# Performance work log

Measured on AMD Instinct MI355X. Metric: run time of the kernel, lower is better.

## Reference

```python
import jax, jax.numpy as jnp
import numpy as np

EPS = 1e-5

def _ln(x, g, b):
    m = x.mean(-1, keepdims=True)
    v = x.var(-1, keepdims=True)
    return (x - m) / jnp.sqrt(v + EPS) * g + b

def _ln_na(x):
    m = x.mean(-1, keepdims=True)
    v = x.var(-1, keepdims=True)
    return (x - m) / jnp.sqrt(v + EPS)

def setup_inputs() -> dict:
    key = jax.random.key(0)
    ks = jax.random.split(key, 12)
    B, J, D, H, E, Z = 128, 4096, 64, 128, 256, 32
    s = 0.05
    return {
        "x": jax.random.normal(ks[0], (B, J), jnp.float32),
        "mask": jax.random.randint(ks[1], (B, J), 0, 2, jnp.int32),
        "feature_embedding": jax.random.normal(ks[2], (J, D), jnp.float32),
        "hW1": jax.random.normal(ks[3], (1 + D, H), jnp.float32) * s,
        "hb1": jnp.zeros((H,), jnp.float32),
        "hg1": jnp.ones((H,), jnp.float32),
        "hbt1": jnp.zeros((H,), jnp.float32),
        "hW2": jax.random.normal(ks[4], (H, D), jnp.float32) * s,
        "hb2": jnp.zeros((D,), jnp.float32),
        "hg2": jnp.ones((D,), jnp.float32),
        "hbt2": jnp.zeros((D,), jnp.float32),
        "eW1": jax.random.normal(ks[5], (D, E), jnp.float32) * s,
        "eb1": jnp.zeros((E,), jnp.float32),
        "eW2": jax.random.normal(ks[6], (E, 2 * Z), jnp.float32) * s,
        "eb2": jnp.zeros((2 * Z,), jnp.float32),
    }

def reference(x, mask, feature_embedding, hW1, hb1, hg1, hbt1, hW2, hb2, hg2, hbt2, eW1, eb1, eW2, eb2):
    B, J = x.shape
    D = feature_embedding.shape[1]
    m = (mask > 0).astype(x.dtype)  # (B, J)
    # per-(b,j) MLP on [x_bj, F_j]; masked entries are zeroed before pooling,
    # which equals the original gather-then-MLP-then-sum over observed entries.
    F = jnp.broadcast_to(feature_embedding[None], (B, J, D))
    h_in = jnp.concatenate([x[..., None], F], axis=-1)        # (B, J, 1+D)
    h = jax.nn.relu(_ln(h_in @ hW1 + hb1, hg1, hbt1))          # (B, J, H)
    h = jax.nn.relu(_ln(h @ hW2 + hb2, hg2, hbt2))             # (B, J, D)
    pooled = jnp.einsum('bjd,bj->bd', h, m)                    # sum over observed
    cnt = jnp.maximum(m.sum(-1, keepdims=True), 1.0)
    c = pooled / cnt                                           # mean pool; zeros if no obs
    # FCLayers (2 layers, LayerNorm w/o affine, ReLU each layer)
    e = jax.nn.relu(_ln_na(c @ eW1 + eb1))                     # (B, E)
    out = jax.nn.relu(_ln_na(e @ eW2 + eb2))                   # (B, 2Z)
    mu, logvar = jnp.split(out, 2, axis=-1)
    return (mu, logvar)
```

## Files before the change

### kernel.cpp

```cpp
#include <hip/hip_runtime.h>
#include <hip/hip_bf16.h>

#define B_  128
#define J_  4096
#define D_  64
#define H_  128
#define E_  256
#define Z_  32

typedef __attribute__((ext_vector_type(8))) short short8;
typedef __attribute__((ext_vector_type(4))) float floatx4;

#define OFF_G      0u
#define OFF_GSTATS 2097152u
#define OFF_SCAL   2162688u
#define OFF_W0C    2162944u
#define OFF_C3     2163456u
#define OFF_W2F    2163968u
#define OFF_POOL   2180352u

#if defined(__has_builtin)
#if __has_builtin(__builtin_amdgcn_cvt_pk_bf16_f32)
#define HAVE_CVT_PK_BF16 1
#endif
#endif

#ifdef HAVE_CVT_PK_BF16
static __device__ __forceinline__ unsigned pk2(float a, float b) {
    return __builtin_bit_cast(unsigned, __builtin_amdgcn_cvt_pk_bf16_f32(a, b));
}
#else
static __device__ __forceinline__ unsigned pk2(float a, float b) {
    __hip_bfloat162 t = __float22bfloat162_rn(make_float2(a, b));
    union { __hip_bfloat162 h; unsigned u; } c; c.h = t; return c.u;
}
#endif

__global__ __launch_bounds__(128) void pre_kernel(
    const float* __restrict__ F, const float* __restrict__ hW1,
    const float* __restrict__ hb1, const float* __restrict__ hg1,
    const float* __restrict__ hbt1, const float* __restrict__ hW2,
    float* __restrict__ Gp, float4* __restrict__ Gstats,
    float* __restrict__ scal, float* __restrict__ w0c, float* __restrict__ c3,
    uint4* __restrict__ w2f, float4* __restrict__ zero4)
{
    __shared__ float red[24];
    const int bid = blockIdx.x;
    const int t = threadIdx.x;

    if (bid > 1024) {
        const int base = (bid - 1025) * 256;
        zero4[base + t]       = make_float4(0.f, 0.f, 0.f, 0.f);
        zero4[base + 128 + t] = make_float4(0.f, 0.f, 0.f, 0.f);
        return;
    }

    if (bid == 1024) {
        const float w0h = hW1[t];
        float s = w0h, q = w0h * w0h;
#pragma unroll
        for (int off = 32; off; off >>= 1) {
            s += __shfl_xor(s, off);
            q += __shfl_xor(q, off);
        }
        if ((t & 63) == 0) { red[(t >> 6) * 2] = s; red[(t >> 6) * 2 + 1] = q; }
        __syncthreads();
        const float mw0  = (red[0] + red[2]) * (1.f / (float)H_);
        const float ew02 = (red[1] + red[3]) * (1.f / (float)H_);
        if (t == 0) { scal[0] = mw0; scal[1] = ew02; }
        w0c[t] = (hW1[t] - mw0) * hg1[t];
        c3[t]  = hbt1[t];

        const int lane = t & 63, half = t >> 6;
        const int quad = lane >> 4, col = lane & 15;
        for (int f = half; f < 16; f += 2) {
            const int kstep = f >> 2, nt = f & 3;
            const int kbase = kstep * 32 + quad * 8;
            const int n = nt * 16 + col;
            unsigned r[4];
#pragma unroll
            for (int p = 0; p < 4; p++)
                r[p] = pk2(hW2[(kbase + 2*p) * D_ + n], hW2[(kbase + 2*p + 1) * D_ + n]);
            w2f[f * 64 + lane] = make_uint4(r[0], r[1], r[2], r[3]);
        }
        return;
    }

    const int j0 = bid * 4;
    const int h  = t;
    const float* f0 = F + (size_t)(j0 + 0) * D_;
    const float* f1 = F + (size_t)(j0 + 1) * D_;
    const float* f2p = F + (size_t)(j0 + 2) * D_;
    const float* f3 = F + (size_t)(j0 + 3) * D_;
    const float bias = hb1[h];
    float a0 = bias, a1 = bias, a2 = bias, a3 = bias;
#pragma unroll
    for (int d = 0; d < D_; d++) {
        const float w = hW1[(d + 1) * H_ + h];
        a0 = fmaf(f0[d], w, a0);
        a1 = fmaf(f1[d], w, a1);
        a2 = fmaf(f2p[d], w, a2);
        a3 = fmaf(f3[d], w, a3);
    }

    const float w0h = hW1[h];
    const float g1h = hg1[h];
    float accs[4] = {a0, a1, a2, a3};
#pragma unroll
    for (int q = 0; q < 4; q++) {
        float s1 = accs[q], s2 = w0h * accs[q], s3 = accs[q] * accs[q];
#pragma unroll
        for (int off = 32; off; off >>= 1) {
            s1 += __shfl_xor(s1, off);
            s2 += __shfl_xor(s2, off);
            s3 += __shfl_xor(s3, off);
        }
        if ((h & 63) == 0) {
            int w = h >> 6;
            red[q*6 + w*3 + 0] = s1; red[q*6 + w*3 + 1] = s2; red[q*6 + w*3 + 2] = s3;
        }
    }
    __syncthreads();
    const float inv = 1.f / (float)H_;
#pragma unroll
    for (int q = 0; q < 4; q++) {
        const float mG = (red[q*6 + 0] + red[q*6 + 3]) * inv;
        if (h == 0)
            Gstats[j0 + q] = make_float4(mG, (red[q*6+1] + red[q*6+4]) * inv,
                                             (red[q*6+2] + red[q*6+5]) * inv, 0.f);
        Gp[(j0 + q) * H_ + h] = (accs[q] - mG) * g1h;
    }
}

#define TPW 2
#define BB  4

__global__ __launch_bounds__(256, 2) void main_kernel(
    const float* __restrict__ x, const int* __restrict__ mask,
    const float* __restrict__ Gp, const float4* __restrict__ Gstats,
    const float* __restrict__ scal,
    const float* __restrict__ w0c, const float* __restrict__ c3,
    const uint4* __restrict__ w2f,
    const float* __restrict__ hb2, const float* __restrict__ hg2,
    const float* __restrict__ hbt2,
    float* __restrict__ pooled)
{
    const int tid  = threadIdx.x;
    const int lane = tid & 63;
    const int wv   = tid >> 6;
    const int quad = lane >> 4;
    const int col  = lane & 15;
    const int b0   = blockIdx.y * BB;

    short8 w2r[16];
#pragma unroll
    for (int f = 0; f < 16; f++) {
        union { uint4 v; short8 s; } c; c.v = w2f[f * 64 + lane];
        w2r[f] = c.s;
    }
    float4 wc[4][2], cc[4][2];
#pragma unroll
    for (int k = 0; k < 4; k++) {
        wc[k][0] = ((const float4*)(w0c + k*32 + quad*8))[0];
        wc[k][1] = ((const float4*)(w0c + k*32 + quad*8))[1];
        cc[k][0] = ((const float4*)(c3  + k*32 + quad*8))[0];
        cc[k][1] = ((const float4*)(c3  + k*32 + quad*8))[1];
    }
    float hb2v[4], g2v[4], bt2v[4];
#pragma unroll
    for (int nt = 0; nt < 4; nt++) {
        hb2v[nt] = hb2[nt*16 + col];
        g2v[nt]  = hg2[nt*16 + col];
        bt2v[nt] = hbt2[nt*16 + col];
    }
    const float mw0s  = scal[0];
    const float ew02s = scal[1];

    float pool[BB][4];
#pragma unroll
    for (int bb = 0; bb < BB; bb++)
#pragma unroll
        for (int nt = 0; nt < 4; nt++) pool[bb][nt] = 0.f;

    for (int t = 0; t < TPW; t++) {
        const int tIdx = (blockIdx.x * 4 + wv) * TPW + t;
        const int j0   = tIdx * 16;
        const int rowA = j0 + col;

        const float4 gs = Gstats[rowA];
        float xv[BB]; int4 mk[BB];
#pragma unroll
        for (int bb = 0; bb < BB; bb++) {
            xv[bb] = x[(size_t)(b0 + bb) * J_ + rowA];
            mk[bb] = *(const int4*)(mask + (size_t)(b0 + bb) * J_ + j0 + quad * 4);
        }
        const float* gpr = Gp + rowA * H_ + quad * 8;
        float4 ga[4][2];
#pragma unroll
        for (int k = 0; k < 4; k++) {
            ga[k][0] = ((const float4*)(gpr + k*32))[0];
            ga[k][1] = ((const float4*)(gpr + k*32))[1];
        }

#pragma unroll
        for (int bb = 0; bb < BB; bb++) {
            const float xA = xv[bb];
            const float mean = fmaf(xA, mw0s, gs.x);
            const float eh2  = fmaf(xA, fmaf(xA, ew02s, 2.f * gs.y), gs.z);
            const float r1   = rsqrtf(fmaf(-mean, mean, eh2) + 1e-5f);

            floatx4 acc[4];
#pragma unroll
            for (int nt = 0; nt < 4; nt++) acc[nt] = (floatx4){0.f, 0.f, 0.f, 0.f};

#pragma unroll
            for (int k = 0; k < 4; k++) {
                const float h0 = fmaxf(0.f, fmaf(fmaf(xA, wc[k][0].x, ga[k][0].x), r1, cc[k][0].x));
                const float h1 = fmaxf(0.f, fmaf(fmaf(xA, wc[k][0].y, ga[k][0].y), r1, cc[k][0].y));
                const float h2 = fmaxf(0.f, fmaf(fmaf(xA, wc[k][0].z, ga[k][0].z), r1, cc[k][0].z));
                const float h3 = fmaxf(0.f, fmaf(fmaf(xA, wc[k][0].w, ga[k][0].w), r1, cc[k][0].w));
                const float h4 = fmaxf(0.f, fmaf(fmaf(xA, wc[k][1].x, ga[k][1].x), r1, cc[k][1].x));
                const float h5 = fmaxf(0.f, fmaf(fmaf(xA, wc[k][1].y, ga[k][1].y), r1, cc[k][1].y));
                const float h6 = fmaxf(0.f, fmaf(fmaf(xA, wc[k][1].z, ga[k][1].z), r1, cc[k][1].z));
                const float h7 = fmaxf(0.f, fmaf(fmaf(xA, wc[k][1].w, ga[k][1].w), r1, cc[k][1].w));
                union { unsigned u[4]; short8 s; } af;
                af.u[0] = pk2(h0, h1);
                af.u[1] = pk2(h2, h3);
                af.u[2] = pk2(h4, h5);
                af.u[3] = pk2(h6, h7);
                acc[0] = __builtin_amdgcn_mfma_f32_16x16x32_bf16(af.s, w2r[k*4+0], acc[0], 0, 0, 0);
                acc[1] = __builtin_amdgcn_mfma_f32_16x16x32_bf16(af.s, w2r[k*4+1], acc[1], 0, 0, 0);
                acc[2] = __builtin_amdgcn_mfma_f32_16x16x32_bf16(af.s, w2r[k*4+2], acc[2], 0, 0, 0);
                acc[3] = __builtin_amdgcn_mfma_f32_16x16x32_bf16(af.s, w2r[k*4+3], acc[3], 0, 0, 0);
            }

            float sa[4], qa[4];
#pragma unroll
            for (int r = 0; r < 4; r++) {
                const float v0 = acc[0][r] + hb2v[0];
                const float v1 = acc[1][r] + hb2v[1];
                const float v2 = acc[2][r] + hb2v[2];
                const float v3 = acc[3][r] + hb2v[3];
                acc[0][r] = v0; acc[1][r] = v1; acc[2][r] = v2; acc[3][r] = v3;
                sa[r] = (v0 + v1) + (v2 + v3);
                qa[r] = fmaf(v0, v0, fmaf(v1, v1, fmaf(v2, v2, v3 * v3)));
            }
#pragma unroll
            for (int m = 1; m < 16; m <<= 1) {
#pragma unroll
                for (int r = 0; r < 4; r++) {
                    sa[r] += __shfl_xor(sa[r], m);
                    qa[r] += __shfl_xor(qa[r], m);
                }
            }
            float mrr[4];
            mrr[0] = (mk[bb].x > 0) ? 1.f : 0.f;
            mrr[1] = (mk[bb].y > 0) ? 1.f : 0.f;
            mrr[2] = (mk[bb].z > 0) ? 1.f : 0.f;
            mrr[3] = (mk[bb].w > 0) ? 1.f : 0.f;
#pragma unroll
            for (int r = 0; r < 4; r++) {
                const float m2 = sa[r] * (1.f / 64.f);
                const float v2 = fmaf(-m2, m2, qa[r] * (1.f / 64.f));
                const float r2 = rsqrtf(v2 + 1e-5f);
#pragma unroll
                for (int nt = 0; nt < 4; nt++) {
                    const float rg  = r2 * g2v[nt];
                    const float off = fmaf(-m2, rg, bt2v[nt]);
                    const float o   = fmaxf(0.f, fmaf(acc[nt][r], rg, off));
                    pool[bb][nt] = fmaf(mrr[r], o, pool[bb][nt]);
                }
            }
        }
    }

#pragma unroll
    for (int m = 16; m < 64; m <<= 1)
#pragma unroll
        for (int bb = 0; bb < BB; bb++)
#pragma unroll
            for (int nt = 0; nt < 4; nt++)
                pool[bb][nt] += __shfl_xor(pool[bb][nt], m);

    if (lane < 16) {
#pragma unroll
        for (int bb = 0; bb < BB; bb++)
#pragma unroll
            for (int nt = 0; nt < 4; nt++)
                atomicAdd(&pooled[(size_t)(b0 + bb) * D_ + nt * 16 + lane], pool[bb][nt]);
    }
}

__global__ __launch_bounds__(256) void final_kernel(
    const float* __restrict__ pooled, const int* __restrict__ mask,
    const float* __restrict__ eW1, const float* __restrict__ eb1,
    const float* __restrict__ eW2, const float* __restrict__ eb2,
    float* __restrict__ out)
{
    __shared__ float c_lds[D_];
    __shared__ float e_lds[E_];
    __shared__ float red[8];
    __shared__ float redc[4];
    const int b = blockIdx.x;
    const int t = threadIdx.x;
    const int lane = t & 63, wid = t >> 6;

    {
        const int4* mrow = (const int4*)(mask + (size_t)b * J_);
        int s = 0;
#pragma unroll
        for (int i = 0; i < 4; i++) {
            const int4 v = mrow[i * 256 + t];
            s += (v.x > 0) + (v.y > 0) + (v.z > 0) + (v.w > 0);
        }
        float fs = (float)s;
#pragma unroll
        for (int off = 32; off; off >>= 1) fs += __shfl_xor(fs, off);
        if (lane == 0) redc[wid] = fs;
    }
    __syncthreads();
    const float cn = fmaxf((redc[0] + redc[1]) + (redc[2] + redc[3]), 1.f);
    if (t < D_) c_lds[t] = pooled[(size_t)b * D_ + t] / cn;
    __syncthreads();

    float acc = eb1[t];
#pragma unroll
    for (int d = 0; d < D_; d++)
        acc = fmaf(c_lds[d], eW1[(size_t)d * E_ + t], acc);

    float s = acc, s2 = acc * acc;
#pragma unroll
    for (int off = 32; off; off >>= 1) {
        s  += __shfl_xor(s, off);
        s2 += __shfl_xor(s2, off);
    }
    if ((t & 63) == 0) { red[wid * 2] = s; red[wid * 2 + 1] = s2; }
    __syncthreads();
    s  = red[0] + red[2] + red[4] + red[6];
    s2 = red[1] + red[3] + red[5] + red[7];
    const float m = s * (1.f / (float)E_);
    const float v = fmaf(-m, m, s2 * (1.f / (float)E_));
    const float r = rsqrtf(v + 1e-5f);
    e_lds[t] = fmaxf(0.f, (acc - m) * r);
    __syncthreads();

    if (t < 64) {
        float a2 = eb2[t];
#pragma unroll 8
        for (int k = 0; k < E_; k++)
            a2 = fmaf(e_lds[k], eW2[(size_t)k * 64 + t], a2);

        float u = a2, u2 = a2 * a2;
#pragma unroll
        for (int off = 32; off; off >>= 1) {
            u  += __shfl_xor(u, off);
            u2 += __shfl_xor(u2, off);
        }
        const float m2 = u * (1.f / 64.f);
        const float v2 = fmaf(-m2, m2, u2 * (1.f / 64.f));
        const float r2 = rsqrtf(v2 + 1e-5f);
        const float o  = fmaxf(0.f, (a2 - m2) * r2);
        if (t < Z_) out[(size_t)b * Z_ + t] = o;
        else        out[(size_t)B_ * Z_ + (size_t)b * Z_ + (t - Z_)] = o;
    }
}

extern "C" void kernel_launch(void* const* d_in, const int* in_sizes, int n_in,
                              void* d_out, int out_size, void* d_ws, size_t ws_size,
                              hipStream_t stream) {
    const float* x    = (const float*)d_in[0];
    const int*   mask = (const int*)d_in[1];
    const float* F    = (const float*)d_in[2];
    const float* hW1  = (const float*)d_in[3];
    const float* hb1  = (const float*)d_in[4];
    const float* hg1  = (const float*)d_in[5];
    const float* hbt1 = (const float*)d_in[6];
    const float* hW2  = (const float*)d_in[7];
    const float* hb2  = (const float*)d_in[8];
    const float* hg2  = (const float*)d_in[9];
    const float* hbt2 = (const float*)d_in[10];
    const float* eW1  = (const float*)d_in[11];
    const float* eb1  = (const float*)d_in[12];
    const float* eW2  = (const float*)d_in[13];
    const float* eb2  = (const float*)d_in[14];
    float* out = (float*)d_out;

    char* ws = (char*)d_ws;
    float*  Gp     = (float*)(ws + OFF_G);
    float4* Gstats = (float4*)(ws + OFF_GSTATS);
    float*  scal   = (float*)(ws + OFF_SCAL);
    float*  w0c    = (float*)(ws + OFF_W0C);
    float*  c3     = (float*)(ws + OFF_C3);
    uint4*  w2f    = (uint4*)(ws + OFF_W2F);
    float*  pooled = (float*)(ws + OFF_POOL);

    pre_kernel<<<1033, 128, 0, stream>>>(F, hW1, hb1, hg1, hbt1, hW2,
                                         Gp, Gstats, scal, w0c, c3, w2f,
                                         (float4*)pooled);
    main_kernel<<<dim3(J_ / (16 * 4 * TPW), B_ / BB), 256, 0, stream>>>(
        x, mask, Gp, Gstats, scal, w0c, c3, w2f, hb2, hg2, hbt2, pooled);
    final_kernel<<<B_, E_, 0, stream>>>(pooled, mask, eW1, eb1, eW2, eb2, out);
}
```

Measured before the change: 138.5 us.

## Use DPP row reductions, packed FP32 FMA, and bf16 packed ReLU across kernels

Replaces shuffle-based wave reductions with DPP row16 adds plus two cross-row shuffles, and packs the hidden-layer affine math into two-wide float FMAs. It also applies ReLU after bf16 packing with a packed 16-bit integer max, vectorizes the feature-embedding loads in the pre kernel, and splits the serial FMA chains in the encoder head into several accumulators for more ILP. The aim is to cut VALU and cross-lane instruction count in the hot MFMA loop. It relies on compiler support for the DPP and elementwise-fma builtins, and on inline asm for the packed max.

```diff
diff --git a/kernel.cpp b/kernel.cpp
--- a/kernel.cpp
+++ b/kernel.cpp
@@ -10,6 +10,7 @@
 
 typedef __attribute__((ext_vector_type(8))) short short8;
 typedef __attribute__((ext_vector_type(4))) float floatx4;
+typedef __attribute__((ext_vector_type(2))) float floatx2;
 
 #define OFF_G      0u
 #define OFF_GSTATS 2097152u
@@ -35,6 +36,42 @@
     union { __hip_bfloat162 h; unsigned u; } c; c.h = t; return c.u;
 }
 #endif
+
+template<int CTRL>
+static __device__ __forceinline__ float dpp_add_(float v) {
+    const int t = __builtin_amdgcn_update_dpp(0, __builtin_bit_cast(int, v),
+                                              CTRL, 0xF, 0xF, true);
+    return v + __builtin_bit_cast(float, t);
+}
+static __device__ __forceinline__ float row16_sum(float v) {
+    v = dpp_add_<0xB1>(v);
+    v = dpp_add_<0x4E>(v);
+    v = dpp_add_<0x124>(v);
+    v = dpp_add_<0x128>(v);
+    return v;
+}
+static __device__ __forceinline__ float wave64_sum(float v) {
+    v = row16_sum(v);
+    v += __shfl_xor(v, 16);
+    v += __shfl_xor(v, 32);
+    return v;
+}
+
+#if defined(__has_builtin) && __has_builtin(__builtin_elementwise_fma)
+static __device__ __forceinline__ floatx2 pkfma(floatx2 a, floatx2 b, floatx2 c) {
+    return __builtin_elementwise_fma(a, b, c);
+}
+#else
+static __device__ __forceinline__ floatx2 pkfma(floatx2 a, floatx2 b, floatx2 c) {
+    return a * b + c;
+}
+#endif
+
+static __device__ __forceinline__ unsigned relu2_bf16(unsigned u) {
+    unsigned d; const unsigned z = 0;
+    asm("v_pk_max_i16 %0, %1, %2" : "=v"(d) : "v"(u), "v"(z));
+    return d;
+}
 
 __global__ __launch_bounds__(128) void pre_kernel(
     const float* __restrict__ F, const float* __restrict__ hW1,
@@ -57,12 +94,8 @@
 
     if (bid == 1024) {
         const float w0h = hW1[t];
-        float s = w0h, q = w0h * w0h;
-#pragma unroll
-        for (int off = 32; off; off >>= 1) {
-            s += __shfl_xor(s, off);
-            q += __shfl_xor(q, off);
-        }
+        const float s = wave64_sum(w0h);
+        const float q = wave64_sum(w0h * w0h);
         if ((t & 63) == 0) { red[(t >> 6) * 2] = s; red[(t >> 6) * 2 + 1] = q; }
         __syncthreads();
         const float mw0  = (red[0] + red[2]) * (1.f / (float)H_);
@@ -88,19 +121,27 @@
 
     const int j0 = bid * 4;
     const int h  = t;
-    const float* f0 = F + (size_t)(j0 + 0) * D_;
-    const float* f1 = F + (size_t)(j0 + 1) * D_;
-    const float* f2p = F + (size_t)(j0 + 2) * D_;
-    const float* f3 = F + (size_t)(j0 + 3) * D_;
+    const float4* f0v = (const float4*)(F + (size_t)(j0 + 0) * D_);
+    const float4* f1v = (const float4*)(F + (size_t)(j0 + 1) * D_);
+    const float4* f2v = (const float4*)(F + (size_t)(j0 + 2) * D_);
+    const float4* f3v = (const float4*)(F + (size_t)(j0 + 3) * D_);
     const float bias = hb1[h];
     float a0 = bias, a1 = bias, a2 = bias, a3 = bias;
 #pragma unroll
-    for (int d = 0; d < D_; d++) {
-        const float w = hW1[(d + 1) * H_ + h];
-        a0 = fmaf(f0[d], w, a0);
-        a1 = fmaf(f1[d], w, a1);
-        a2 = fmaf(f2p[d], w, a2);
-        a3 = fmaf(f3[d], w, a3);
+    for (int dq = 0; dq < 16; dq++) {
+        const float4 q0 = f0v[dq], q1 = f1v[dq], q2 = f2v[dq], q3 = f3v[dq];
+        const float wa = hW1[(4*dq + 1) * H_ + h];
+        const float wb = hW1[(4*dq + 2) * H_ + h];
+        const float wc = hW1[(4*dq + 3) * H_ + h];
+        const float wd = hW1[(4*dq + 4) * H_ + h];
+        a0 = fmaf(q0.x, wa, a0); a0 = fmaf(q0.y, wb, a0);
+        a0 = fmaf(q0.z, wc, a0); a0 = fmaf(q0.w, wd, a0);
+        a1 = fmaf(q1.x, wa, a1); a1 = fmaf(q1.y, wb, a1);
+        a1 = fmaf(q1.z, wc, a1); a1 = fmaf(q1.w, wd, a1);
+        a2 = fmaf(q2.x, wa, a2); a2 = fmaf(q2.y, wb, a2);
+        a2 = fmaf(q2.z, wc, a2); a2 = fmaf(q2.w, wd, a2);
+        a3 = fmaf(q3.x, wa, a3); a3 = fmaf(q3.y, wb, a3);
+        a3 = fmaf(q3.z, wc, a3); a3 = fmaf(q3.w, wd, a3);
     }
 
     const float w0h = hW1[h];
@@ -108,13 +149,9 @@
     float accs[4] = {a0, a1, a2, a3};
 #pragma unroll
     for (int q = 0; q < 4; q++) {
-        float s1 = accs[q], s2 = w0h * accs[q], s3 = accs[q] * accs[q];
-#pragma unroll
-        for (int off = 32; off; off >>= 1) {
-            s1 += __shfl_xor(s1, off);
-            s2 += __shfl_xor(s2, off);
-            s3 += __shfl_xor(s3, off);
-        }
+        const float s1 = wave64_sum(accs[q]);
+        const float s2 = wave64_sum(w0h * accs[q]);
+        const float s3 = wave64_sum(accs[q] * accs[q]);
         if ((h & 63) == 0) {
             int w = h >> 6;
             red[q*6 + w*3 + 0] = s1; red[q*6 + w*3 + 1] = s2; red[q*6 + w*3 + 2] = s3;
@@ -158,18 +195,20 @@
         union { uint4 v; short8 s; } c; c.v = w2f[f * 64 + lane];
         w2r[f] = c.s;
     }
-    float4 wc[4][2], cc[4][2];
+    floatx2 wc2[4][4], cc2[4][4];
 #pragma unroll
     for (int k = 0; k < 4; k++) {
-        wc[k][0] = ((const float4*)(w0c + k*32 + quad*8))[0];
-        wc[k][1] = ((const float4*)(w0c + k*32 + quad*8))[1];
-        cc[k][0] = ((const float4*)(c3  + k*32 + quad*8))[0];
-        cc[k][1] = ((const float4*)(c3  + k*32 + quad*8))[1];
-    }
-    float hb2v[4], g2v[4], bt2v[4];
+        const floatx2* wp = (const floatx2*)(w0c + k*32 + quad*8);
+        const floatx2* cp = (const floatx2*)(c3  + k*32 + quad*8);
+#pragma unroll
+        for (int p = 0; p < 4; p++) { wc2[k][p] = wp[p]; cc2[k][p] = cp[p]; }
+    }
+    floatx2 b2p[4];
+    float g2v[4], bt2v[4];
 #pragma unroll
     for (int nt = 0; nt < 4; nt++) {
-        hb2v[nt] = hb2[nt*16 + col];
+        const float hb = hb2[nt*16 + col];
+        b2p[nt] = (floatx2){hb, hb};
         g2v[nt]  = hg2[nt*16 + col];
         bt2v[nt] = hbt2[nt*16 + col];
     }
@@ -195,11 +234,12 @@
             mk[bb] = *(const int4*)(mask + (size_t)(b0 + bb) * J_ + j0 + quad * 4);
         }
         const float* gpr = Gp + rowA * H_ + quad * 8;
-        float4 ga[4][2];
+        floatx2 ga2[4][4];
 #pragma unroll
         for (int k = 0; k < 4; k++) {
-            ga[k][0] = ((const float4*)(gpr + k*32))[0];
-            ga[k][1] = ((const float4*)(gpr + k*32))[1];
+            const floatx2* gp2 = (const floatx2*)(gpr + k*32);
+#pragma unroll
+            for (int p = 0; p < 4; p++) ga2[k][p] = gp2[p];
         }
 
 #pragma unroll
@@ -208,6 +248,8 @@
             const float mean = fmaf(xA, mw0s, gs.x);
             const float eh2  = fmaf(xA, fmaf(xA, ew02s, 2.f * gs.y), gs.z);
             const float r1   = rsqrtf(fmaf(-mean, mean, eh2) + 1e-5f);
+            const floatx2 xAp = (floatx2){xA, xA};
+            const floatx2 r1p = (floatx2){r1, r1};
 
             floatx4 acc[4];
 #pragma unroll
@@ -215,43 +257,41 @@
 
 #pragma unroll
             for (int k = 0; k < 4; k++) {
-                const float h0 = fmaxf(0.f, fmaf(fmaf(xA, wc[k][0].x, ga[k][0].x), r1, cc[k][0].x));
-                const float h1 = fmaxf(0.f, fmaf(fmaf(xA, wc[k][0].y, ga[k][0].y), r1, cc[k][0].y));
-                const float h2 = fmaxf(0.f, fmaf(fmaf(xA, wc[k][0].z, ga[k][0].z), r1, cc[k][0].z));
-                const float h3 = fmaxf(0.f, fmaf(fmaf(xA, wc[k][0].w, ga[k][0].w), r1, cc[k][0].w));
-                const float h4 = fmaxf(0.f, fmaf(fmaf(xA, wc[k][1].x, ga[k][1].x), r1, cc[k][1].x));
-                const float h5 = fmaxf(0.f, fmaf(fmaf(xA, wc[k][1].y, ga[k][1].y), r1, cc[k][1].y));
-                const float h6 = fmaxf(0.f, fmaf(fmaf(xA, wc[k][1].z, ga[k][1].z), r1, cc[k][1].z));
-                const float h7 = fmaxf(0.f, fmaf(fmaf(xA, wc[k][1].w, ga[k][1].w), r1, cc[k][1].w));
                 union { unsigned u[4]; short8 s; } af;
-                af.u[0] = pk2(h0, h1);
-                af.u[1] = pk2(h2, h3);
-                af.u[2] = pk2(h4, h5);
-                af.u[3] = pk2(h6, h7);
+#pragma unroll
+                for (int p = 0; p < 4; p++) {
+                    const floatx2 tv = pkfma(pkfma(xAp, wc2[k][p], ga2[k][p]), r1p, cc2[k][p]);
+                    af.u[p] = relu2_bf16(pk2(tv.x, tv.y));
+                }
                 acc[0] = __builtin_amdgcn_mfma_f32_16x16x32_bf16(af.s, w2r[k*4+0], acc[0], 0, 0, 0);
                 acc[1] = __builtin_amdgcn_mfma_f32_16x16x32_bf16(af.s, w2r[k*4+1], acc[1], 0, 0, 0);
                 acc[2] = __builtin_amdgcn_mfma_f32_16x16x32_bf16(af.s, w2r[k*4+2], acc[2], 0, 0, 0);
                 acc[3] = __builtin_amdgcn_mfma_f32_16x16x32_bf16(af.s, w2r[k*4+3], acc[3], 0, 0, 0);
             }
 
-            float sa[4], qa[4];
+            floatx2 vb[4][2];
+#pragma unroll
+            for (int nt = 0; nt < 4; nt++) {
+                const floatx2 a01 = (floatx2){acc[nt][0], acc[nt][1]};
+                const floatx2 a23 = (floatx2){acc[nt][2], acc[nt][3]};
+                vb[nt][0] = a01 + b2p[nt];
+                vb[nt][1] = a23 + b2p[nt];
+            }
+            floatx2 sap[2], qap[2];
+#pragma unroll
+            for (int rp = 0; rp < 2; rp++) {
+                sap[rp] = (vb[0][rp] + vb[1][rp]) + (vb[2][rp] + vb[3][rp]);
+                qap[rp] = pkfma(vb[3][rp], vb[3][rp],
+                          pkfma(vb[2][rp], vb[2][rp],
+                          pkfma(vb[1][rp], vb[1][rp],
+                          vb[0][rp] * vb[0][rp])));
+            }
+            float sa[4] = {sap[0].x, sap[0].y, sap[1].x, sap[1].y};
+            float qa[4] = {qap[0].x, qap[0].y, qap[1].x, qap[1].y};
 #pragma unroll
             for (int r = 0; r < 4; r++) {
-                const float v0 = acc[0][r] + hb2v[0];
-                const float v1 = acc[1][r] + hb2v[1];
-                const float v2 = acc[2][r] + hb2v[2];
-                const float v3 = acc[3][r] + hb2v[3];
-                acc[0][r] = v0; acc[1][r] = v1; acc[2][r] = v2; acc[3][r] = v3;
-                sa[r] = (v0 + v1) + (v2 + v3);
-                qa[r] = fmaf(v0, v0, fmaf(v1, v1, fmaf(v2, v2, v3 * v3)));
-            }
-#pragma unroll
-            for (int m = 1; m < 16; m <<= 1) {
-#pragma unroll
-                for (int r = 0; r < 4; r++) {
-                    sa[r] += __shfl_xor(sa[r], m);
-                    qa[r] += __shfl_xor(qa[r], m);
-                }
+                sa[r] = row16_sum(sa[r]);
+                qa[r] = row16_sum(qa[r]);
             }
             float mrr[4];
             mrr[0] = (mk[bb].x > 0) ? 1.f : 0.f;
@@ -265,9 +305,10 @@
                 const float r2 = rsqrtf(v2 + 1e-5f);
 #pragma unroll
                 for (int nt = 0; nt < 4; nt++) {
+                    const float vv  = (r & 1) ? vb[nt][r >> 1].y : vb[nt][r >> 1].x;
                     const float rg  = r2 * g2v[nt];
                     const float off = fmaf(-m2, rg, bt2v[nt]);
-                    const float o   = fmaxf(0.f, fmaf(acc[nt][r], rg, off));
+                    const float o   = fmaxf(0.f, fmaf(vv, rg, off));
                     pool[bb][nt] = fmaf(mrr[r], o, pool[bb][nt]);
                 }
             }
@@ -313,9 +354,7 @@
             const int4 v = mrow[i * 256 + t];
             s += (v.x > 0) + (v.y > 0) + (v.z > 0) + (v.w > 0);
         }
-        float fs = (float)s;
-#pragma unroll
-        for (int off = 32; off; off >>= 1) fs += __shfl_xor(fs, off);
+        const float fs = wave64_sum((float)s);
         if (lane == 0) redc[wid] = fs;
     }
     __syncthreads();
@@ -323,39 +362,46 @@
     if (t < D_) c_lds[t] = pooled[(size_t)b * D_ + t] / cn;
     __syncthreads();
 
-    float acc = eb1[t];
-#pragma unroll
-    for (int d = 0; d < D_; d++)
-        acc = fmaf(c_lds[d], eW1[(size_t)d * E_ + t], acc);
-
-    float s = acc, s2 = acc * acc;
-#pragma unroll
-    for (int off = 32; off; off >>= 1) {
-        s  += __shfl_xor(s, off);
-        s2 += __shfl_xor(s2, off);
-    }
+    float p0 = eb1[t], p1 = 0.f, p2 = 0.f, p3 = 0.f;
+#pragma unroll
+    for (int d = 0; d < D_; d += 4) {
+        p0 = fmaf(c_lds[d + 0], eW1[(size_t)(d + 0) * E_ + t], p0);
+        p1 = fmaf(c_lds[d + 1], eW1[(size_t)(d + 1) * E_ + t], p1);
+        p2 = fmaf(c_lds[d + 2], eW1[(size_t)(d + 2) * E_ + t], p2);
+        p3 = fmaf(c_lds[d + 3], eW1[(size_t)(d + 3) * E_ + t], p3);
+    }
+    const float acc = (p0 + p1) + (p2 + p3);
+
+    const float s  = wave64_sum(acc);
+    const float s2 = wave64_sum(acc * acc);
     if ((t & 63) == 0) { red[wid * 2] = s; red[wid * 2 + 1] = s2; }
     __syncthreads();
-    s  = red[0] + red[2] + red[4] + red[6];
-    s2 = red[1] + red[3] + red[5] + red[7];
-    const float m = s * (1.f / (float)E_);
-    const float v = fmaf(-m, m, s2 * (1.f / (float)E_));
+    const float ts  = red[0] + red[2] + red[4] + red[6];
+    const float ts2 = red[1] + red[3] + red[5] + red[7];
+    const float m = ts * (1.f / (float)E_);
+    const float v = fmaf(-m, m, ts2 * (1.f / (float)E_));
     const float r = rsqrtf(v + 1e-5f);
     e_lds[t] = fmaxf(0.f, (acc - m) * r);
     __syncthreads();
 
     if (t < 64) {
-        float a2 = eb2[t];
-#pragma unroll 8
-        for (int k = 0; k < E_; k++)
-            a2 = fmaf(e_lds[k], eW2[(size_t)k * 64 + t], a2);
-
-        float u = a2, u2 = a2 * a2;
-#pragma unroll
-        for (int off = 32; off; off >>= 1) {
-            u  += __shfl_xor(u, off);
-            u2 += __shfl_xor(u2, off);
-        }
+        float q0 = eb2[t], q1 = 0.f, q2 = 0.f, q3 = 0.f,
+              q4 = 0.f, q5 = 0.f, q6 = 0.f, q7 = 0.f;
+#pragma unroll
+        for (int k = 0; k < E_; k += 8) {
+            q0 = fmaf(e_lds[k + 0], eW2[(size_t)(k + 0) * 64 + t], q0);
+            q1 = fmaf(e_lds[k + 1], eW2[(size_t)(k + 1) * 64 + t], q1);
+            q2 = fmaf(e_lds[k + 2], eW2[(size_t)(k + 2) * 64 + t], q2);
+            q3 = fmaf(e_lds[k + 3], eW2[(size_t)(k + 3) * 64 + t], q3);
+            q4 = fmaf(e_lds[k + 4], eW2[(size_t)(k + 4) * 64 + t], q4);
+            q5 = fmaf(e_lds[k + 5], eW2[(size_t)(k + 5) * 64 + t], q5);
+            q6 = fmaf(e_lds[k + 6], eW2[(size_t)(k + 6) * 64 + t], q6);
+            q7 = fmaf(e_lds[k + 7], eW2[(size_t)(k + 7) * 64 + t], q7);
+        }
+        const float a2 = ((q0 + q1) + (q2 + q3)) + ((q4 + q5) + (q6 + q7));
+
+        const float u  = wave64_sum(a2);
+        const float u2 = wave64_sum(a2 * a2);
         const float m2 = u * (1.f / 64.f);
         const float v2 = fmaf(-m2, m2, u2 * (1.f / 64.f));
         const float r2 = rsqrtf(v2 + 1e-5f);
```

New measurement: 123.8 us, median of 2. 1.12x faster.
